# Optimization experiments

Measured on AMD Instinct MI355X. Metric: run time of the kernel, lower is better.

## Reference

```python
import jax, jax.numpy as jnp
import numpy as np

NUM_LINKS = 1048576


def _euler_rots(theta):
    # theta: [N,3] -> per-link rotation R = Rz @ Ry @ Rx, shape [N,3,3]
    cx, cy, cz = jnp.cos(theta[:, 0]), jnp.cos(theta[:, 1]), jnp.cos(theta[:, 2])
    sx, sy, sz = jnp.sin(theta[:, 0]), jnp.sin(theta[:, 1]), jnp.sin(theta[:, 2])
    z = jnp.zeros_like(cx)
    o = jnp.ones_like(cx)
    rx = jnp.stack([jnp.stack([o, z, z], -1),
                    jnp.stack([z, cx, -sx], -1),
                    jnp.stack([z, sx, cx], -1)], -2)
    ry = jnp.stack([jnp.stack([cy, z, sy], -1),
                    jnp.stack([z, o, z], -1),
                    jnp.stack([-sy, z, cy], -1)], -2)
    rz = jnp.stack([jnp.stack([cz, -sz, z], -1),
                    jnp.stack([sz, cz, z], -1),
                    jnp.stack([z, z, o], -1)], -2)
    return jnp.matmul(rz, jnp.matmul(ry, rx))  # [N,3,3]


def setup_inputs() -> dict:
    key = jax.random.key(0)
    k1, k2 = jax.random.split(key)
    link_lengths = jax.random.uniform(k1, (NUM_LINKS,), dtype=jnp.float32)
    theta = jax.random.normal(k2, (NUM_LINKS, 3), dtype=jnp.float32)
    return {"link_lengths": link_lengths, "theta": theta}


def reference(link_lengths, theta):
    # Original loop computes eff_pos_i = sum_{j=0..i} (R_0 @ R_1 @ ... @ R_j) @ t_j
    # with t_j = l_j * e_z. Vectorize via prefix matrix products + cumsum.
    R = _euler_rots(theta)                                   # [N,3,3]
    P = jax.lax.associative_scan(jnp.matmul, R)              # P_j = R_0@...@R_j
    v = P[:, :, 2] * link_lengths[:, None]                   # P_j @ (l_j * e_z)
    return jnp.cumsum(v, axis=0)                             # [N,3]
```

## Files before the change

### kernel.cpp

```cpp
#include <hip/hip_runtime.h>
#include <math.h>


#define TPB 256
#define EPT 4
#define EPB (TPB * EPT)
#define MAXB 1024
#define NWAVE (TPB / 64)

struct Xf {
    float m[9];
    float p[3];
};

__device__ __forceinline__ void xf_identity(Xf& x) {
    x.m[0] = 1.f; x.m[1] = 0.f; x.m[2] = 0.f;
    x.m[3] = 0.f; x.m[4] = 1.f; x.m[5] = 0.f;
    x.m[6] = 0.f; x.m[7] = 0.f; x.m[8] = 1.f;
    x.p[0] = 0.f; x.p[1] = 0.f; x.p[2] = 0.f;
}

__device__ __forceinline__ Xf xf_comb(const Xf& A, const Xf& B) {
    Xf o;
#pragma unroll
    for (int r = 0; r < 3; ++r) {
        const float a0 = A.m[r * 3 + 0], a1 = A.m[r * 3 + 1], a2 = A.m[r * 3 + 2];
#pragma unroll
        for (int c = 0; c < 3; ++c) {
            o.m[r * 3 + c] = a0 * B.m[0 * 3 + c] + a1 * B.m[1 * 3 + c] + a2 * B.m[2 * 3 + c];
        }
        o.p[r] = A.p[r] + a0 * B.p[0] + a1 * B.p[1] + a2 * B.p[2];
    }
    return o;
}

__device__ __forceinline__ void xf_fold(Xf& a, float ax, float ay, float az, float l) {
    float sx, cx, sy, cy, sz, cz;
    sincosf(ax, &sx, &cx);
    sincosf(ay, &sy, &cy);
    sincosf(az, &sz, &cz);
    const float sysx = sy * sx, sycx = sy * cx;
    const float r00 = cz * cy;
    const float r01 = cz * sysx - sz * cx;
    const float r02 = sz * sx + cz * sycx;
    const float r10 = sz * cy;
    const float r11 = cz * cx + sz * sysx;
    const float r12 = sz * sycx - cz * sx;
    const float r20 = -sy;
    const float r21 = cy * sx;
    const float r22 = cy * cx;
    const float t0 = l * r02, t1 = l * r12, t2 = l * r22;
    const float p0 = a.p[0] + a.m[0] * t0 + a.m[1] * t1 + a.m[2] * t2;
    const float p1 = a.p[1] + a.m[3] * t0 + a.m[4] * t1 + a.m[5] * t2;
    const float p2 = a.p[2] + a.m[6] * t0 + a.m[7] * t1 + a.m[8] * t2;
    const float n0 = a.m[0] * r00 + a.m[1] * r10 + a.m[2] * r20;
    const float n1 = a.m[0] * r01 + a.m[1] * r11 + a.m[2] * r21;
    const float n2 = a.m[0] * r02 + a.m[1] * r12 + a.m[2] * r22;
    const float n3 = a.m[3] * r00 + a.m[4] * r10 + a.m[5] * r20;
    const float n4 = a.m[3] * r01 + a.m[4] * r11 + a.m[5] * r21;
    const float n5 = a.m[3] * r02 + a.m[4] * r12 + a.m[5] * r22;
    const float n6 = a.m[6] * r00 + a.m[7] * r10 + a.m[8] * r20;
    const float n7 = a.m[6] * r01 + a.m[7] * r11 + a.m[8] * r21;
    const float n8 = a.m[6] * r02 + a.m[7] * r12 + a.m[8] * r22;
    a.m[0] = n0; a.m[1] = n1; a.m[2] = n2;
    a.m[3] = n3; a.m[4] = n4; a.m[5] = n5;
    a.m[6] = n6; a.m[7] = n7; a.m[8] = n8;
    a.p[0] = p0; a.p[1] = p1; a.p[2] = p2;
}

__device__ __forceinline__ Xf xf_shfl_up(const Xf& a, int delta) {
    Xf o;
#pragma unroll
    for (int k = 0; k < 9; ++k) o.m[k] = __shfl_up(a.m[k], delta, 64);
#pragma unroll
    for (int k = 0; k < 3; ++k) o.p[k] = __shfl_up(a.p[k], delta, 64);
    return o;
}
__device__ __forceinline__ Xf xf_shfl_down(const Xf& a, int delta) {
    Xf o;
#pragma unroll
    for (int k = 0; k < 9; ++k) o.m[k] = __shfl_down(a.m[k], delta, 64);
#pragma unroll
    for (int k = 0; k < 3; ++k) o.p[k] = __shfl_down(a.p[k], delta, 64);
    return o;
}

__device__ __forceinline__ Xf wave_scan(Xf a, int lane) {
#pragma unroll
    for (int off = 1; off < 64; off <<= 1) {
        const Xf b = xf_shfl_up(a, off);
        if (lane >= off) a = xf_comb(b, a);
    }
    return a;
}

__device__ __forceinline__ Xf wave_reduce(Xf v, int lane) {
#pragma unroll
    for (int off = 1; off < 64; off <<= 1) {
        const Xf b = xf_shfl_down(v, off);
        if (lane + off < 64) v = xf_comb(v, b);
    }
    return v;
}

__device__ __forceinline__ Xf xf_load4(const Xf* p) {
    const float4* g = (const float4*)p;
    const float4 x = g[0], y = g[1], z = g[2];
    Xf b;
    b.m[0] = x.x; b.m[1] = x.y; b.m[2] = x.z;
    b.m[3] = x.w; b.m[4] = y.x; b.m[5] = y.y;
    b.m[6] = y.z; b.m[7] = y.w; b.m[8] = z.x;
    b.p[0] = z.y; b.p[1] = z.z; b.p[2] = z.w;
    return b;
}
__device__ __forceinline__ void xf_store4(Xf* p, const Xf& b) {
    float4* g = (float4*)p;
    g[0] = make_float4(b.m[0], b.m[1], b.m[2], b.m[3]);
    g[1] = make_float4(b.m[4], b.m[5], b.m[6], b.m[7]);
    g[2] = make_float4(b.m[8], b.p[0], b.p[1], b.p[2]);
}

__device__ __forceinline__ void local_fold(const float* __restrict__ ll,
                                           const float* __restrict__ th,
                                           long long j0, int n, Xf& a,
                                           float pe[EPT][3]) {
    xf_identity(a);
    if (j0 + EPT <= n) {
        const float4* th4 = (const float4*)(th + 3 * j0);
        const float4 A = th4[0], B = th4[1], C = th4[2];
        const float4 L = *(const float4*)(ll + j0);
        xf_fold(a, A.x, A.y, A.z, L.x);
        pe[0][0] = a.p[0]; pe[0][1] = a.p[1]; pe[0][2] = a.p[2];
        xf_fold(a, A.w, B.x, B.y, L.y);
        pe[1][0] = a.p[0]; pe[1][1] = a.p[1]; pe[1][2] = a.p[2];
        xf_fold(a, B.z, B.w, C.x, L.z);
        pe[2][0] = a.p[0]; pe[2][1] = a.p[1]; pe[2][2] = a.p[2];
        xf_fold(a, C.y, C.z, C.w, L.w);
        pe[3][0] = a.p[0]; pe[3][1] = a.p[1]; pe[3][2] = a.p[2];
    } else {
#pragma unroll
        for (int e = 0; e < EPT; ++e) {
            const long long j = j0 + e;
            if (j < n) xf_fold(a, th[3 * j + 0], th[3 * j + 1], th[3 * j + 2], ll[j]);
            pe[e][0] = a.p[0]; pe[e][1] = a.p[1]; pe[e][2] = a.p[2];
        }
    }
}

__device__ __forceinline__ void write_out(float* __restrict__ out, long long j0, int n,
                                          const Xf& T, const float pe[EPT][3]) {
    if (j0 + EPT <= n) {
        float o[EPT * 3];
#pragma unroll
        for (int e = 0; e < EPT; ++e) {
            const float q0 = pe[e][0], q1 = pe[e][1], q2 = pe[e][2];
            o[e * 3 + 0] = T.p[0] + T.m[0] * q0 + T.m[1] * q1 + T.m[2] * q2;
            o[e * 3 + 1] = T.p[1] + T.m[3] * q0 + T.m[4] * q1 + T.m[5] * q2;
            o[e * 3 + 2] = T.p[2] + T.m[6] * q0 + T.m[7] * q1 + T.m[8] * q2;
        }
        float4* o4 = (float4*)(out + 3 * j0);
        o4[0] = make_float4(o[0], o[1], o[2], o[3]);
        o4[1] = make_float4(o[4], o[5], o[6], o[7]);
        o4[2] = make_float4(o[8], o[9], o[10], o[11]);
    } else {
#pragma unroll
        for (int e = 0; e < EPT; ++e) {
            const long long j = j0 + e;
            if (j < n) {
                const float q0 = pe[e][0], q1 = pe[e][1], q2 = pe[e][2];
                out[3 * j + 0] = T.p[0] + T.m[0] * q0 + T.m[1] * q1 + T.m[2] * q2;
                out[3 * j + 1] = T.p[1] + T.m[3] * q0 + T.m[4] * q1 + T.m[5] * q2;
                out[3 * j + 2] = T.p[2] + T.m[6] * q0 + T.m[7] * q1 + T.m[8] * q2;
            }
        }
    }
}

__global__ void __launch_bounds__(TPB) fk_agg(const float* __restrict__ ll,
                                              const float* __restrict__ th,
                                              Xf* __restrict__ agg, int n) {
    __shared__ Xf wagg[NWAVE];
    const int t = threadIdx.x;
    const int lane = t & 63, w = t >> 6;
    const long long j0 = (long long)blockIdx.x * EPB + (long long)t * EPT;

    Xf a;
    float pe[EPT][3];
    local_fold(ll, th, j0, n, a, pe);

    const Xf red = wave_reduce(a, lane);
    if (lane == 0) wagg[w] = red;
    __syncthreads();

    if (t == 0) {
        Xf acc = wagg[0];
#pragma unroll
        for (int k = 1; k < NWAVE; ++k) acc = xf_comb(acc, wagg[k]);
        xf_store4(&agg[blockIdx.x], acc);
    }
}

__global__ void __launch_bounds__(TPB) fk_apply(const float* __restrict__ ll,
                                                const float* __restrict__ th,
                                                const Xf* __restrict__ agg,
                                                float* __restrict__ out, int n) {
    __shared__ Xf wred[NWAVE];
    __shared__ Xf wagg[NWAVE];
    __shared__ Xf shG;
    const int t = threadIdx.x, bid = blockIdx.x;
    const int lane = t & 63, w = t >> 6;
    const long long j0 = (long long)bid * EPB + (long long)t * EPT;

    {
        const int i0 = t * EPT;
        Xf A;
        xf_identity(A);
#pragma unroll
        for (int e = 0; e < EPT; ++e) {
            const int i = i0 + e;
            if (i < bid) A = xf_comb(A, xf_load4(&agg[i]));
        }
        const Xf red = wave_reduce(A, lane);
        if (lane == 0) wred[w] = red;
    }
    __syncthreads();
    if (t == 0) {
        Xf G = wred[0];
#pragma unroll
        for (int k = 1; k < NWAVE; ++k) G = xf_comb(G, wred[k]);
        shG = G;
    }

    Xf a;
    float pe[EPT][3];
    local_fold(ll, th, j0, n, a, pe);

    const Xf inc = wave_scan(a, lane);
    if (lane == 63) wagg[w] = inc;
    __syncthreads();

    Xf exw;
    xf_identity(exw);
    for (int k = 0; k < w; ++k) exw = xf_comb(exw, wagg[k]);

    const Xf ext = xf_shfl_up(inc, 1);

    Xf T = xf_comb(shG, exw);
    if (lane != 0) T = xf_comb(T, ext);

    write_out(out, j0, n, T, pe);
}

extern "C" void kernel_launch(void* const* d_in, const int* in_sizes, int n_in,
                              void* d_out, int out_size, void* d_ws, size_t ws_size,
                              hipStream_t stream) {
    const float* ll = (const float*)d_in[0];
    const float* th = (const float*)d_in[1];
    float* out = (float*)d_out;
    const int n = in_sizes[0];

    int nb = (n + EPB - 1) / EPB;
    if (nb > MAXB) nb = MAXB;

    Xf* agg = (Xf*)d_ws;

    fk_agg<<<nb, TPB, 0, stream>>>(ll, th, agg, n);
    fk_apply<<<nb, TPB, 0, stream>>>(ll, th, agg, out, n);
}
```

Baseline: 30.83 us.

## Switch to scan-then-propagate: local scan writes partial outputs, fixup applies block prefix

The first kernel now does the full intra-block scan of the per-link transforms. It writes block-local end-effector positions straight to the output and stores the block aggregates. The second kernel no longer re-reads theta or recomputes the trig and the scan. It only combines earlier block aggregates and applies the resulting prefix transform to the stored outputs in place. This removes the duplicated sin/cos, fold and wave-scan work, at the cost of an extra read-modify-write pass over the output buffer. The first kernel also changes to 512 threads with 2 elements per thread.

```diff
diff --git a/kernel.cpp b/kernel.cpp
--- a/kernel.cpp
+++ b/kernel.cpp
@@ -2,11 +2,15 @@
 #include <math.h>
 
 
-#define TPB 256
-#define EPT 4
-#define EPB (TPB * EPT)
+#define K1_TPB 512
+#define K1_EPT 2
+#define K1_EPB (K1_TPB * K1_EPT)
+#define K1_NW (K1_TPB / 64)
+#define K2_TPB 256
+#define K2_EPT 4
+#define K2_EPB (K2_TPB * K2_EPT)
 #define MAXB 1024
-#define NWAVE (TPB / 64)
+#define EPG (MAXB / K2_TPB)
 
 struct Xf {
     float m[9];
@@ -120,103 +124,89 @@
     g[2] = make_float4(b.m[8], b.p[0], b.p[1], b.p[2]);
 }
 
-__device__ __forceinline__ void local_fold(const float* __restrict__ ll,
-                                           const float* __restrict__ th,
-                                           long long j0, int n, Xf& a,
-                                           float pe[EPT][3]) {
+__device__ __forceinline__ void xf_apply(const Xf& T, float q0, float q1, float q2,
+                                         float& o0, float& o1, float& o2) {
+    o0 = T.p[0] + T.m[0] * q0 + T.m[1] * q1 + T.m[2] * q2;
+    o1 = T.p[1] + T.m[3] * q0 + T.m[4] * q1 + T.m[5] * q2;
+    o2 = T.p[2] + T.m[6] * q0 + T.m[7] * q1 + T.m[8] * q2;
+}
+
+__global__ void __launch_bounds__(K1_TPB, 6)
+fk_local(const float* __restrict__ ll, const float* __restrict__ th,
+         Xf* __restrict__ agg, float* __restrict__ out, int n) {
+    __shared__ Xf wagg[K1_NW];
+    const int t = threadIdx.x, bid = blockIdx.x;
+    const int lane = t & 63, w = t >> 6;
+    const long long j0 = (long long)bid * K1_EPB + (long long)t * K1_EPT;
+
+    Xf a;
     xf_identity(a);
-    if (j0 + EPT <= n) {
-        const float4* th4 = (const float4*)(th + 3 * j0);
-        const float4 A = th4[0], B = th4[1], C = th4[2];
-        const float4 L = *(const float4*)(ll + j0);
-        xf_fold(a, A.x, A.y, A.z, L.x);
+    float pe[K1_EPT][3];
+    if (j0 + K1_EPT <= n) {
+        const float2* th2 = (const float2*)(th + 3 * j0);
+        const float2 d0 = th2[0], d1 = th2[1], d2 = th2[2];
+        const float2 L = *(const float2*)(ll + j0);
+        xf_fold(a, d0.x, d0.y, d1.x, L.x);
         pe[0][0] = a.p[0]; pe[0][1] = a.p[1]; pe[0][2] = a.p[2];
-        xf_fold(a, A.w, B.x, B.y, L.y);
+        xf_fold(a, d1.y, d2.x, d2.y, L.y);
         pe[1][0] = a.p[0]; pe[1][1] = a.p[1]; pe[1][2] = a.p[2];
-        xf_fold(a, B.z, B.w, C.x, L.z);
-        pe[2][0] = a.p[0]; pe[2][1] = a.p[1]; pe[2][2] = a.p[2];
-        xf_fold(a, C.y, C.z, C.w, L.w);
-        pe[3][0] = a.p[0]; pe[3][1] = a.p[1]; pe[3][2] = a.p[2];
     } else {
 #pragma unroll
-        for (int e = 0; e < EPT; ++e) {
+        for (int e = 0; e < K1_EPT; ++e) {
             const long long j = j0 + e;
             if (j < n) xf_fold(a, th[3 * j + 0], th[3 * j + 1], th[3 * j + 2], ll[j]);
             pe[e][0] = a.p[0]; pe[e][1] = a.p[1]; pe[e][2] = a.p[2];
         }
     }
-}
-
-__device__ __forceinline__ void write_out(float* __restrict__ out, long long j0, int n,
-                                          const Xf& T, const float pe[EPT][3]) {
-    if (j0 + EPT <= n) {
-        float o[EPT * 3];
-#pragma unroll
-        for (int e = 0; e < EPT; ++e) {
-            const float q0 = pe[e][0], q1 = pe[e][1], q2 = pe[e][2];
-            o[e * 3 + 0] = T.p[0] + T.m[0] * q0 + T.m[1] * q1 + T.m[2] * q2;
-            o[e * 3 + 1] = T.p[1] + T.m[3] * q0 + T.m[4] * q1 + T.m[5] * q2;
-            o[e * 3 + 2] = T.p[2] + T.m[6] * q0 + T.m[7] * q1 + T.m[8] * q2;
-        }
-        float4* o4 = (float4*)(out + 3 * j0);
-        o4[0] = make_float4(o[0], o[1], o[2], o[3]);
-        o4[1] = make_float4(o[4], o[5], o[6], o[7]);
-        o4[2] = make_float4(o[8], o[9], o[10], o[11]);
+
+    const Xf inc = wave_scan(a, lane);
+    if (lane == 63) wagg[w] = inc;
+    __syncthreads();
+
+    Xf exw;
+    xf_identity(exw);
+    for (int k = 0; k < w; ++k) exw = xf_comb(exw, wagg[k]);
+
+    if (t == K1_TPB - 1) xf_store4(&agg[bid], xf_comb(exw, inc));
+
+    const Xf ext = xf_shfl_up(inc, 1);
+    Xf T = exw;
+    if (lane != 0) T = xf_comb(T, ext);
+
+    if (j0 + K1_EPT <= n) {
+        float o0, o1, o2, o3, o4, o5;
+        xf_apply(T, pe[0][0], pe[0][1], pe[0][2], o0, o1, o2);
+        xf_apply(T, pe[1][0], pe[1][1], pe[1][2], o3, o4, o5);
+        float2* q2 = (float2*)(out + 3 * j0);
+        q2[0] = make_float2(o0, o1);
+        q2[1] = make_float2(o2, o3);
+        q2[2] = make_float2(o4, o5);
     } else {
 #pragma unroll
-        for (int e = 0; e < EPT; ++e) {
+        for (int e = 0; e < K1_EPT; ++e) {
             const long long j = j0 + e;
             if (j < n) {
-                const float q0 = pe[e][0], q1 = pe[e][1], q2 = pe[e][2];
-                out[3 * j + 0] = T.p[0] + T.m[0] * q0 + T.m[1] * q1 + T.m[2] * q2;
-                out[3 * j + 1] = T.p[1] + T.m[3] * q0 + T.m[4] * q1 + T.m[5] * q2;
-                out[3 * j + 2] = T.p[2] + T.m[6] * q0 + T.m[7] * q1 + T.m[8] * q2;
+                float o0, o1, o2;
+                xf_apply(T, pe[e][0], pe[e][1], pe[e][2], o0, o1, o2);
+                out[3 * j + 0] = o0; out[3 * j + 1] = o1; out[3 * j + 2] = o2;
             }
         }
     }
 }
 
-__global__ void __launch_bounds__(TPB) fk_agg(const float* __restrict__ ll,
-                                              const float* __restrict__ th,
-                                              Xf* __restrict__ agg, int n) {
-    __shared__ Xf wagg[NWAVE];
-    const int t = threadIdx.x;
-    const int lane = t & 63, w = t >> 6;
-    const long long j0 = (long long)blockIdx.x * EPB + (long long)t * EPT;
-
-    Xf a;
-    float pe[EPT][3];
-    local_fold(ll, th, j0, n, a, pe);
-
-    const Xf red = wave_reduce(a, lane);
-    if (lane == 0) wagg[w] = red;
-    __syncthreads();
-
-    if (t == 0) {
-        Xf acc = wagg[0];
-#pragma unroll
-        for (int k = 1; k < NWAVE; ++k) acc = xf_comb(acc, wagg[k]);
-        xf_store4(&agg[blockIdx.x], acc);
-    }
-}
-
-__global__ void __launch_bounds__(TPB) fk_apply(const float* __restrict__ ll,
-                                                const float* __restrict__ th,
-                                                const Xf* __restrict__ agg,
-                                                float* __restrict__ out, int n) {
-    __shared__ Xf wred[NWAVE];
-    __shared__ Xf wagg[NWAVE];
+__global__ void __launch_bounds__(K2_TPB)
+fk_fixup(const Xf* __restrict__ agg, float* __restrict__ out, int n, int nb) {
+    __shared__ Xf wred[K2_TPB / 64];
     __shared__ Xf shG;
     const int t = threadIdx.x, bid = blockIdx.x;
     const int lane = t & 63, w = t >> 6;
-    const long long j0 = (long long)bid * EPB + (long long)t * EPT;
 
     {
-        const int i0 = t * EPT;
+        const int i0 = t * EPG;
         Xf A;
         xf_identity(A);
 #pragma unroll
-        for (int e = 0; e < EPT; ++e) {
+        for (int e = 0; e < EPG; ++e) {
             const int i = i0 + e;
             if (i < bid) A = xf_comb(A, xf_load4(&agg[i]));
         }
@@ -227,28 +217,35 @@
     if (t == 0) {
         Xf G = wred[0];
 #pragma unroll
-        for (int k = 1; k < NWAVE; ++k) G = xf_comb(G, wred[k]);
+        for (int k = 1; k < K2_TPB / 64; ++k) G = xf_comb(G, wred[k]);
         shG = G;
     }
-
-    Xf a;
-    float pe[EPT][3];
-    local_fold(ll, th, j0, n, a, pe);
-
-    const Xf inc = wave_scan(a, lane);
-    if (lane == 63) wagg[w] = inc;
     __syncthreads();
-
-    Xf exw;
-    xf_identity(exw);
-    for (int k = 0; k < w; ++k) exw = xf_comb(exw, wagg[k]);
-
-    const Xf ext = xf_shfl_up(inc, 1);
-
-    Xf T = xf_comb(shG, exw);
-    if (lane != 0) T = xf_comb(T, ext);
-
-    write_out(out, j0, n, T, pe);
+    const Xf G = shG;
+
+    const long long j0 = (long long)bid * K2_EPB + (long long)t * K2_EPT;
+    if (j0 + K2_EPT <= n) {
+        float4* o4 = (float4*)(out + 3 * j0);
+        const float4 x = o4[0], y = o4[1], z = o4[2];
+        float r[12];
+        xf_apply(G, x.x, x.y, x.z, r[0], r[1], r[2]);
+        xf_apply(G, x.w, y.x, y.y, r[3], r[4], r[5]);
+        xf_apply(G, y.z, y.w, z.x, r[6], r[7], r[8]);
+        xf_apply(G, z.y, z.z, z.w, r[9], r[10], r[11]);
+        o4[0] = make_float4(r[0], r[1], r[2], r[3]);
+        o4[1] = make_float4(r[4], r[5], r[6], r[7]);
+        o4[2] = make_float4(r[8], r[9], r[10], r[11]);
+    } else {
+#pragma unroll
+        for (int e = 0; e < K2_EPT; ++e) {
+            const long long j = j0 + e;
+            if (j < n) {
+                float o0, o1, o2;
+                xf_apply(G, out[3 * j + 0], out[3 * j + 1], out[3 * j + 2], o0, o1, o2);
+                out[3 * j + 0] = o0; out[3 * j + 1] = o1; out[3 * j + 2] = o2;
+            }
+        }
+    }
 }
 
 extern "C" void kernel_launch(void* const* d_in, const int* in_sizes, int n_in,
@@ -259,11 +256,11 @@
     float* out = (float*)d_out;
     const int n = in_sizes[0];
 
-    int nb = (n + EPB - 1) / EPB;
+    int nb = (n + K1_EPB - 1) / K1_EPB;
     if (nb > MAXB) nb = MAXB;
 
     Xf* agg = (Xf*)d_ws;
 
-    fk_agg<<<nb, TPB, 0, stream>>>(ll, th, agg, n);
-    fk_apply<<<nb, TPB, 0, stream>>>(ll, th, agg, out, n);
-}
+    fk_local<<<nb, K1_TPB, 0, stream>>>(ll, th, agg, out, n);
+    fk_fixup<<<nb, K2_TPB, 0, stream>>>(agg, out, n, nb);
+}
```

Result: faster. 29.80 us (-3.3%).

## Use DPP wave scan and polynomial sincos in forward-kinematics kernels

Applied to the files above, without the earlier changes.

Swaps library sincosf for a custom Cody-Waite range reduction plus minimax polynomial, which drops the slow large-argument path. The shuffle-based wave scan and reduce are replaced by a DPP row_shr/row_bcast scan that uses identity fill values. The reduction is now taken from lane 63 of the inclusive scan. Launch bounds gain an occupancy hint, and the agg kernel no longer records per-element positions. Accuracy for large angles relies on the simple two-term reduction.

```diff
diff --git a/kernel.cpp b/kernel.cpp
--- a/kernel.cpp
+++ b/kernel.cpp
@@ -34,11 +34,33 @@
     return o;
 }
 
+__device__ __forceinline__ void fast_sincos(float x, float& s, float& c) {
+    const float fn = __builtin_rintf(x * 0.636619772367581343f);
+    const int n = (int)fn;
+    float r = __builtin_fmaf(fn, -1.57079637050628662109375f, x);
+    r = __builtin_fmaf(fn, 4.37113900018624283e-8f, r);
+    const float r2 = r * r;
+    float sp = __builtin_fmaf(r2, -1.9515295891e-4f, 8.3321608736e-3f);
+    sp = __builtin_fmaf(r2, sp, -1.6666654611e-1f);
+    const float ss = __builtin_fmaf(r * r2, sp, r);
+    float cp = __builtin_fmaf(r2, 2.443315711809948e-5f, -1.388731625493765e-3f);
+    cp = __builtin_fmaf(r2, cp, 4.166664568298827e-2f);
+    const float cc = __builtin_fmaf(r2 * r2, cp,
+                                    __builtin_fmaf(r2, -0.5f, 1.0f));
+    const int q = n & 3;
+    const float s0 = (q & 1) ? cc : ss;
+    const float c0 = (q & 1) ? ss : cc;
+    const unsigned sgn_s = (unsigned)(q & 2) << 30;
+    const unsigned sgn_c = (unsigned)((q + 1) & 2) << 30;
+    s = __uint_as_float(__float_as_uint(s0) ^ sgn_s);
+    c = __uint_as_float(__float_as_uint(c0) ^ sgn_c);
+}
+
 __device__ __forceinline__ void xf_fold(Xf& a, float ax, float ay, float az, float l) {
     float sx, cx, sy, cy, sz, cz;
-    sincosf(ax, &sx, &cx);
-    sincosf(ay, &sy, &cy);
-    sincosf(az, &sz, &cz);
+    fast_sincos(ax, sx, cx);
+    fast_sincos(ay, sy, cy);
+    fast_sincos(az, sz, cz);
     const float sysx = sy * sx, sycx = sy * cx;
     const float r00 = cz * cy;
     const float r01 = cz * sysx - sz * cx;
@@ -68,39 +90,47 @@
     a.p[0] = p0; a.p[1] = p1; a.p[2] = p2;
 }
 
-__device__ __forceinline__ Xf xf_shfl_up(const Xf& a, int delta) {
+template <int CTRL, int RMASK>
+__device__ __forceinline__ float dpp_f(float src, float oldv) {
+    return __int_as_float(__builtin_amdgcn_update_dpp(
+        __float_as_int(oldv), __float_as_int(src), CTRL, RMASK, 0xF, false));
+}
+
+template <int CTRL, int RMASK>
+__device__ __forceinline__ Xf xf_scan_step(const Xf& v) {
+    Xf b;
+    b.m[0] = dpp_f<CTRL, RMASK>(v.m[0], 1.f);
+    b.m[1] = dpp_f<CTRL, RMASK>(v.m[1], 0.f);
+    b.m[2] = dpp_f<CTRL, RMASK>(v.m[2], 0.f);
+    b.m[3] = dpp_f<CTRL, RMASK>(v.m[3], 0.f);
+    b.m[4] = dpp_f<CTRL, RMASK>(v.m[4], 1.f);
+    b.m[5] = dpp_f<CTRL, RMASK>(v.m[5], 0.f);
+    b.m[6] = dpp_f<CTRL, RMASK>(v.m[6], 0.f);
+    b.m[7] = dpp_f<CTRL, RMASK>(v.m[7], 0.f);
+    b.m[8] = dpp_f<CTRL, RMASK>(v.m[8], 1.f);
+    b.p[0] = dpp_f<CTRL, RMASK>(v.p[0], 0.f);
+    b.p[1] = dpp_f<CTRL, RMASK>(v.p[1], 0.f);
+    b.p[2] = dpp_f<CTRL, RMASK>(v.p[2], 0.f);
+    return xf_comb(b, v);
+}
+
+__device__ __forceinline__ Xf wave_scan(Xf v) {
+    v = xf_scan_step<0x111, 0xF>(v);
+    v = xf_scan_step<0x112, 0xF>(v);
+    v = xf_scan_step<0x114, 0xF>(v);
+    v = xf_scan_step<0x118, 0xF>(v);
+    v = xf_scan_step<0x142, 0xA>(v);
+    v = xf_scan_step<0x143, 0xC>(v);
+    return v;
+}
+
+__device__ __forceinline__ Xf xf_shfl_up1(const Xf& a) {
     Xf o;
 #pragma unroll
-    for (int k = 0; k < 9; ++k) o.m[k] = __shfl_up(a.m[k], delta, 64);
-#pragma unroll
-    for (int k = 0; k < 3; ++k) o.p[k] = __shfl_up(a.p[k], delta, 64);
+    for (int k = 0; k < 9; ++k) o.m[k] = __shfl_up(a.m[k], 1, 64);
+#pragma unroll
+    for (int k = 0; k < 3; ++k) o.p[k] = __shfl_up(a.p[k], 1, 64);
     return o;
-}
-__device__ __forceinline__ Xf xf_shfl_down(const Xf& a, int delta) {
-    Xf o;
-#pragma unroll
-    for (int k = 0; k < 9; ++k) o.m[k] = __shfl_down(a.m[k], delta, 64);
-#pragma unroll
-    for (int k = 0; k < 3; ++k) o.p[k] = __shfl_down(a.p[k], delta, 64);
-    return o;
-}
-
-__device__ __forceinline__ Xf wave_scan(Xf a, int lane) {
-#pragma unroll
-    for (int off = 1; off < 64; off <<= 1) {
-        const Xf b = xf_shfl_up(a, off);
-        if (lane >= off) a = xf_comb(b, a);
-    }
-    return a;
-}
-
-__device__ __forceinline__ Xf wave_reduce(Xf v, int lane) {
-#pragma unroll
-    for (int off = 1; off < 64; off <<= 1) {
-        const Xf b = xf_shfl_down(v, off);
-        if (lane + off < 64) v = xf_comb(v, b);
-    }
-    return v;
 }
 
 __device__ __forceinline__ Xf xf_load4(const Xf* p) {
@@ -120,65 +150,43 @@
     g[2] = make_float4(b.m[8], b.p[0], b.p[1], b.p[2]);
 }
 
+__device__ __forceinline__ void xf_apply(const Xf& T, float q0, float q1, float q2,
+                                         float& o0, float& o1, float& o2) {
+    o0 = T.p[0] + T.m[0] * q0 + T.m[1] * q1 + T.m[2] * q2;
+    o1 = T.p[1] + T.m[3] * q0 + T.m[4] * q1 + T.m[5] * q2;
+    o2 = T.p[2] + T.m[6] * q0 + T.m[7] * q1 + T.m[8] * q2;
+}
+
 __device__ __forceinline__ void local_fold(const float* __restrict__ ll,
                                            const float* __restrict__ th,
                                            long long j0, int n, Xf& a,
-                                           float pe[EPT][3]) {
+                                           float pe[EPT][3], bool record) {
     xf_identity(a);
     if (j0 + EPT <= n) {
         const float4* th4 = (const float4*)(th + 3 * j0);
         const float4 A = th4[0], B = th4[1], C = th4[2];
         const float4 L = *(const float4*)(ll + j0);
         xf_fold(a, A.x, A.y, A.z, L.x);
-        pe[0][0] = a.p[0]; pe[0][1] = a.p[1]; pe[0][2] = a.p[2];
+        if (record) { pe[0][0] = a.p[0]; pe[0][1] = a.p[1]; pe[0][2] = a.p[2]; }
         xf_fold(a, A.w, B.x, B.y, L.y);
-        pe[1][0] = a.p[0]; pe[1][1] = a.p[1]; pe[1][2] = a.p[2];
+        if (record) { pe[1][0] = a.p[0]; pe[1][1] = a.p[1]; pe[1][2] = a.p[2]; }
         xf_fold(a, B.z, B.w, C.x, L.z);
-        pe[2][0] = a.p[0]; pe[2][1] = a.p[1]; pe[2][2] = a.p[2];
+        if (record) { pe[2][0] = a.p[0]; pe[2][1] = a.p[1]; pe[2][2] = a.p[2]; }
         xf_fold(a, C.y, C.z, C.w, L.w);
-        pe[3][0] = a.p[0]; pe[3][1] = a.p[1]; pe[3][2] = a.p[2];
+        if (record) { pe[3][0] = a.p[0]; pe[3][1] = a.p[1]; pe[3][2] = a.p[2]; }
     } else {
 #pragma unroll
         for (int e = 0; e < EPT; ++e) {
             const long long j = j0 + e;
             if (j < n) xf_fold(a, th[3 * j + 0], th[3 * j + 1], th[3 * j + 2], ll[j]);
-            pe[e][0] = a.p[0]; pe[e][1] = a.p[1]; pe[e][2] = a.p[2];
-        }
-    }
-}
-
-__device__ __forceinline__ void write_out(float* __restrict__ out, long long j0, int n,
-                                          const Xf& T, const float pe[EPT][3]) {
-    if (j0 + EPT <= n) {
-        float o[EPT * 3];
-#pragma unroll
-        for (int e = 0; e < EPT; ++e) {
-            const float q0 = pe[e][0], q1 = pe[e][1], q2 = pe[e][2];
-            o[e * 3 + 0] = T.p[0] + T.m[0] * q0 + T.m[1] * q1 + T.m[2] * q2;
-            o[e * 3 + 1] = T.p[1] + T.m[3] * q0 + T.m[4] * q1 + T.m[5] * q2;
-            o[e * 3 + 2] = T.p[2] + T.m[6] * q0 + T.m[7] * q1 + T.m[8] * q2;
-        }
-        float4* o4 = (float4*)(out + 3 * j0);
-        o4[0] = make_float4(o[0], o[1], o[2], o[3]);
-        o4[1] = make_float4(o[4], o[5], o[6], o[7]);
-        o4[2] = make_float4(o[8], o[9], o[10], o[11]);
-    } else {
-#pragma unroll
-        for (int e = 0; e < EPT; ++e) {
-            const long long j = j0 + e;
-            if (j < n) {
-                const float q0 = pe[e][0], q1 = pe[e][1], q2 = pe[e][2];
-                out[3 * j + 0] = T.p[0] + T.m[0] * q0 + T.m[1] * q1 + T.m[2] * q2;
-                out[3 * j + 1] = T.p[1] + T.m[3] * q0 + T.m[4] * q1 + T.m[5] * q2;
-                out[3 * j + 2] = T.p[2] + T.m[6] * q0 + T.m[7] * q1 + T.m[8] * q2;
-            }
-        }
-    }
-}
-
-__global__ void __launch_bounds__(TPB) fk_agg(const float* __restrict__ ll,
-                                              const float* __restrict__ th,
-                                              Xf* __restrict__ agg, int n) {
+            if (record) { pe[e][0] = a.p[0]; pe[e][1] = a.p[1]; pe[e][2] = a.p[2]; }
+        }
+    }
+}
+
+__global__ void __launch_bounds__(TPB, 4)
+fk_agg(const float* __restrict__ ll, const float* __restrict__ th,
+       Xf* __restrict__ agg, int n) {
     __shared__ Xf wagg[NWAVE];
     const int t = threadIdx.x;
     const int lane = t & 63, w = t >> 6;
@@ -186,10 +194,10 @@
 
     Xf a;
     float pe[EPT][3];
-    local_fold(ll, th, j0, n, a, pe);
-
-    const Xf red = wave_reduce(a, lane);
-    if (lane == 0) wagg[w] = red;
+    local_fold(ll, th, j0, n, a, pe, false);
+
+    const Xf inc = wave_scan(a);
+    if (lane == 63) wagg[w] = inc;
     __syncthreads();
 
     if (t == 0) {
@@ -200,10 +208,9 @@
     }
 }
 
-__global__ void __launch_bounds__(TPB) fk_apply(const float* __restrict__ ll,
-                                                const float* __restrict__ th,
-                                                const Xf* __restrict__ agg,
-                                                float* __restrict__ out, int n) {
+__global__ void __launch_bounds__(TPB, 4)
+fk_apply(const float* __restrict__ ll, const float* __restrict__ th,
+         const Xf* __restrict__ agg, float* __restrict__ out, int n) {
     __shared__ Xf wred[NWAVE];
     __shared__ Xf wagg[NWAVE];
     __shared__ Xf shG;
@@ -220,8 +227,8 @@
             const int i = i0 + e;
             if (i < bid) A = xf_comb(A, xf_load4(&agg[i]));
         }
-        const Xf red = wave_reduce(A, lane);
-        if (lane == 0) wred[w] = red;
+        const Xf inc = wave_scan(A);
+        if (lane == 63) wred[w] = inc;
     }
     __syncthreads();
     if (t == 0) {
@@ -233,9 +240,9 @@
 
     Xf a;
     float pe[EPT][3];
-    local_fold(ll, th, j0, n, a, pe);
-
-    const Xf inc = wave_scan(a, lane);
+    local_fold(ll, th, j0, n, a, pe, true);
+
+    const Xf inc = wave_scan(a);
     if (lane == 63) wagg[w] = inc;
     __syncthreads();
 
@@ -243,12 +250,32 @@
     xf_identity(exw);
     for (int k = 0; k < w; ++k) exw = xf_comb(exw, wagg[k]);
 
-    const Xf ext = xf_shfl_up(inc, 1);
+    const Xf ext = xf_shfl_up1(inc);
 
     Xf T = xf_comb(shG, exw);
     if (lane != 0) T = xf_comb(T, ext);
 
-    write_out(out, j0, n, T, pe);
+    if (j0 + EPT <= n) {
+        float o[EPT * 3];
+#pragma unroll
+        for (int e = 0; e < EPT; ++e)
+            xf_apply(T, pe[e][0], pe[e][1], pe[e][2],
+                     o[e * 3 + 0], o[e * 3 + 1], o[e * 3 + 2]);
+        float4* o4 = (float4*)(out + 3 * j0);
+        o4[0] = make_float4(o[0], o[1], o[2], o[3]);
+        o4[1] = make_float4(o[4], o[5], o[6], o[7]);
+        o4[2] = make_float4(o[8], o[9], o[10], o[11]);
+    } else {
+#pragma unroll
+        for (int e = 0; e < EPT; ++e) {
+            const long long j = j0 + e;
+            if (j < n) {
+                float o0, o1, o2;
+                xf_apply(T, pe[e][0], pe[e][1], pe[e][2], o0, o1, o2);
+                out[3 * j + 0] = o0; out[3 * j + 1] = o1; out[3 * j + 2] = o2;
+            }
+        }
+    }
 }
 
 extern "C" void kernel_launch(void* const* d_in, const int* in_sizes, int n_in,
```

Result: faster. 29.66 us, median of 2 (-3.8%).
